# Performance work log

Hardware: AMD Instinct MI355X
Metric: run time of the kernel (lower is better)

Reference implementation:

```python
import jax, jax.numpy as jnp
import numpy as np

BRANCH = 8
DEPTH = 4
BATCH = 8192


def _build_tree(b=BRANCH, depth=DEPTH):
    level_sizes = [b ** l for l in range(depth + 1)]
    offsets = np.cumsum([0] + level_sizes)
    E = int(offsets[-1])  # 4681 total nodes (edges)
    parent = np.full(E, -1, dtype=np.int64)
    for l in range(1, depth + 1):
        idx = np.arange(level_sizes[l])
        parent[offsets[l] + idx] = offsets[l - 1] + idx // b
    # Each node's softmax group = its parent's children group; root -> group 0 ('ROOT').
    # Internal nodes occupy indices [0, offsets[depth]), so group id = parent+1.
    seg = np.where(parent < 0, 0, parent + 1).astype(np.int32)
    # path_onehot[i, j] = 1 iff j is an ancestor of i or i itself (path to root)
    P = np.zeros((E, E), dtype=np.float32)
    rows = np.arange(E)
    cur = rows.copy()
    for _ in range(depth + 1):
        P[rows, cur] = 1.0
        cur = np.where(parent[cur] < 0, cur, parent[cur])
    P[rows, cur] = 1.0  # root
    return seg, P


def setup_inputs() -> dict:
    key = jax.random.key(0)
    seg, P = _build_tree()
    E = seg.shape[0]
    inputs = jax.random.normal(key, (BATCH, E), dtype=jnp.float32)
    return {
        "inputs": inputs,
        "segment_ids": jnp.asarray(seg),
        "path_onehot": jnp.asarray(P),
    }


def _cascade_log_softmax(inputs, segment_ids, num_segments):
    # inputs: [B, E]; segmented (per-group) log_softmax along the edge axis.
    xT = inputs.T  # [E, B]
    mx = jax.ops.segment_max(xT, segment_ids, num_segments=num_segments)  # [S, B]
    shifted = xT - mx[segment_ids]
    lse = jnp.log(jax.ops.segment_sum(jnp.exp(shifted), segment_ids,
                                      num_segments=num_segments))  # [S, B]
    return (shifted - lse[segment_ids]).T  # [B, E]


def reference(inputs, segment_ids, path_onehot):
    # final_probabilities: product of conditionals along root-to-node paths
    num_segments = int(jnp.max(segment_ids)) + 1
    log_prob = _cascade_log_softmax(inputs, segment_ids, num_segments)  # [B, E]
    # log p(node) = sum of conditional log-probs over ancestors-or-self
    return jnp.exp(log_prob @ path_onehot.T)  # [B, E]
```

## Files before the change

kernel.cpp:

```cpp
#include <hip/hip_runtime.h>


constexpr int E     = 4681;
constexpr int NG    = 585;
constexpr int NSLOT = 5266;

__device__ __forceinline__ int xslot(int i) { return 9 * (i >> 3) + (i & 7); }

__device__ __forceinline__ void async_ld(const float* g, float* l) {
    __builtin_amdgcn_global_load_lds(
        (const __attribute__((address_space(1))) void*)g,
        (__attribute__((address_space(3))) void*)l, 4, 0, 0);
}

__device__ __forceinline__ float group_adj(const float w[8]) {
    float m = w[0];
    #pragma unroll
    for (int k = 1; k < 8; ++k) m = fmaxf(m, w[k]);
    float s = 0.0f;
    #pragma unroll
    for (int k = 0; k < 8; ++k) s += __expf(w[k] - m);
    return -m - __logf(s);
}

__device__ __forceinline__ void rdwin(const float* xs, int g, float w[8]) {
    const float* b = xs + 9 * g;
    #pragma unroll
    for (int k = 0; k < 7; ++k) w[k] = b[1 + k];
    w[7] = b[9];
}

__device__ __forceinline__ float walkD(const float* xs, int g, float adjv) {
    float D = adjv;
    if (g > 0) {
        const int p = (g - 1) >> 3;
        D += xs[xslot(g)] + xs[9 * p + 8];
        if (p > 0) {
            const int pp = (p - 1) >> 3;
            D += xs[xslot(p)] + xs[9 * pp + 8];
            if (pp > 0) D += xs[xslot(pp)] + xs[8];
        }
    }
    return D;
}

template<int S>
__device__ __forceinline__ void emit(float* __restrict__ rout, const float* xs,
                                     int g, float D) {
    float y[8];
    {
        const float* b = xs + 9 * g;
        #pragma unroll
        for (int k = 0; k < 7; ++k) y[k] = __expf(b[1 + k] + D);
        y[7] = __expf(b[9] + D);
    }
    float* q = rout + 8 * g + 1;
    if (S == 0) {
        *(float4*)(q)     = make_float4(y[0], y[1], y[2], y[3]);
        *(float4*)(q + 4) = make_float4(y[4], y[5], y[6], y[7]);
    } else if (S == 1) {
        q[0] = y[0];
        *(float2*)(q + 1) = make_float2(y[1], y[2]);
        *(float4*)(q + 3) = make_float4(y[3], y[4], y[5], y[6]);
        q[7] = y[7];
    } else if (S == 2) {
        *(float2*)(q)     = make_float2(y[0], y[1]);
        *(float4*)(q + 2) = make_float4(y[2], y[3], y[4], y[5]);
        *(float2*)(q + 6) = make_float2(y[6], y[7]);
    } else {
        q[0] = y[0];
        *(float4*)(q + 1) = make_float4(y[1], y[2], y[3], y[4]);
        *(float2*)(q + 5) = make_float2(y[5], y[6]);
        q[7] = y[7];
    }
}

template<int S>
__device__ __forceinline__ void row_body(const float* __restrict__ rin,
                                         float* __restrict__ rout,
                                         float* xs, int tid) {
    const int lbase = tid & ~63;
    #pragma unroll
    for (int j = 0; j < 21; ++j) {
        const int s = 256 * j + tid;
        if (s < NSLOT && (s % 9) != 8) {
            async_ld(rin + 8 * (s / 9) + (s % 9), xs + 256 * j + lbase);
        }
    }
    asm volatile("s_waitcnt vmcnt(0)" ::: "memory");
    __syncthreads();

    const int g0 = tid, g1 = tid + 256, g2 = tid + 512;
    const bool h2 = (g2 < NG);
    float w[8];
    rdwin(xs, g0, w);
    const float a0 = group_adj(w);
    rdwin(xs, g1, w);
    const float a1 = group_adj(w);
    float a2 = 0.f;
    if (h2) { rdwin(xs, g2, w); a2 = group_adj(w); }
    xs[9 * g0 + 8] = a0;
    xs[9 * g1 + 8] = a1;
    if (h2) xs[9 * g2 + 8] = a2;
    __syncthreads();

    emit<S>(rout, xs, g0, walkD(xs, g0, a0));
    emit<S>(rout, xs, g1, walkD(xs, g1, a1));
    if (h2) emit<S>(rout, xs, g2, walkD(xs, g2, a2));
    if (tid == 0) rout[0] = 1.0f;
}

__global__ __launch_bounds__(256, 7) void cascade_kernel(const float* __restrict__ in,
                                                         float* __restrict__ out) {
    __shared__ float xs[NSLOT];
    const int tid = threadIdx.x;
    const long long rowbase = (long long)blockIdx.x * (long long)E;
    const float* rin = in + rowbase;
    float* rout = out + rowbase;
    switch ((int)((rowbase + 1) & 3)) {
        case 0: row_body<0>(rin, rout, xs, tid); break;
        case 1: row_body<1>(rin, rout, xs, tid); break;
        case 2: row_body<2>(rin, rout, xs, tid); break;
        case 3: row_body<3>(rin, rout, xs, tid); break;
    }
}

extern "C" void kernel_launch(void* const* d_in, const int* in_sizes, int n_in,
                              void* d_out, int out_size, void* d_ws, size_t ws_size,
                              hipStream_t stream) {
    const float* in = (const float*)d_in[0];
    float* out = (float*)d_out;
    const int B = in_sizes[0] / E;
    cascade_kernel<<<B, 256, 0, stream>>>(in, out);
}
```

Baseline: 297.2 us.

## Use persistent blocks with double-buffered async LDS prefetch of next row

Switches from one block per row to a persistent grid of 768 blocks that loop over rows, staging the next row into a second LDS buffer while computing the current one. The goal is to hide global load latency and cut per-block launch overhead. The staging index arithmetic is now incremental and branch-free, using dummy loads for padding slots. It trades occupancy (launch bounds 7 to 3, double LDS) for overlap, and relies on vmcnt counting being correct. The store-alignment template is keyed on block id, which matches the row because GRID is a multiple of 4.

```diff
diff --git a/kernel.cpp b/kernel.cpp
--- a/kernel.cpp
+++ b/kernel.cpp
@@ -4,6 +4,8 @@
 constexpr int E     = 4681;
 constexpr int NG    = 585;
 constexpr int NSLOT = 5266;
+constexpr int BUF   = 5376;
+constexpr int GRID  = 768;
 
 __device__ __forceinline__ int xslot(int i) { return 9 * (i >> 3) + (i & 7); }
 
@@ -11,6 +13,22 @@
     __builtin_amdgcn_global_load_lds(
         (const __attribute__((address_space(1))) void*)g,
         (__attribute__((address_space(3))) void*)l, 4, 0, 0);
+}
+
+__device__ __forceinline__ void stage(const float* __restrict__ rin, float* xb,
+                                      int tid, int q0, int r0) {
+    const int lbase = tid & ~63;
+    int off = 8 * q0 + r0;
+    int r = r0;
+    #pragma unroll
+    for (int j = 0; j < 21; ++j) {
+        int a = (r == 8) ? (off - 1) : off;
+        if (j == 20) a = (tid < NSLOT - 5120) ? a : 0;
+        async_ld(rin + a, xb + 256 * j + lbase);
+        const bool wrap = (r >= 5);
+        off += wrap ? 227 : 228;
+        r   += wrap ? -5 : 4;
+    }
 }
 
 __device__ __forceinline__ float group_adj(const float w[8]) {
@@ -76,52 +94,61 @@
 }
 
 template<int S>
-__device__ __forceinline__ void row_body(const float* __restrict__ rin,
-                                         float* __restrict__ rout,
-                                         float* xs, int tid) {
-    const int lbase = tid & ~63;
-    #pragma unroll
-    for (int j = 0; j < 21; ++j) {
-        const int s = 256 * j + tid;
-        if (s < NSLOT && (s % 9) != 8) {
-            async_ld(rin + 8 * (s / 9) + (s % 9), xs + 256 * j + lbase);
-        }
-    }
-    asm volatile("s_waitcnt vmcnt(0)" ::: "memory");
-    __syncthreads();
-
+__device__ __forceinline__ void compute_row(float* xb, float* __restrict__ rout,
+                                            int tid) {
     const int g0 = tid, g1 = tid + 256, g2 = tid + 512;
     const bool h2 = (g2 < NG);
     float w[8];
-    rdwin(xs, g0, w);
-    const float a0 = group_adj(w);
-    rdwin(xs, g1, w);
-    const float a1 = group_adj(w);
+    rdwin(xb, g0, w); const float a0 = group_adj(w);
+    rdwin(xb, g1, w); const float a1 = group_adj(w);
     float a2 = 0.f;
-    if (h2) { rdwin(xs, g2, w); a2 = group_adj(w); }
-    xs[9 * g0 + 8] = a0;
-    xs[9 * g1 + 8] = a1;
-    if (h2) xs[9 * g2 + 8] = a2;
-    __syncthreads();
-
-    emit<S>(rout, xs, g0, walkD(xs, g0, a0));
-    emit<S>(rout, xs, g1, walkD(xs, g1, a1));
-    if (h2) emit<S>(rout, xs, g2, walkD(xs, g2, a2));
+    if (h2) { rdwin(xb, g2, w); a2 = group_adj(w); }
+    xb[9 * g0 + 8] = a0;
+    xb[9 * g1 + 8] = a1;
+    if (h2) xb[9 * g2 + 8] = a2;
+    asm volatile("s_waitcnt lgkmcnt(0)" ::: "memory");
+    __builtin_amdgcn_sched_barrier(0);
+    __builtin_amdgcn_s_barrier();
+    __builtin_amdgcn_sched_barrier(0);
+    emit<S>(rout, xb, g0, walkD(xb, g0, a0));
+    emit<S>(rout, xb, g1, walkD(xb, g1, a1));
+    if (h2) emit<S>(rout, xb, g2, walkD(xb, g2, a2));
     if (tid == 0) rout[0] = 1.0f;
 }
 
-__global__ __launch_bounds__(256, 7) void cascade_kernel(const float* __restrict__ in,
-                                                         float* __restrict__ out) {
-    __shared__ float xs[NSLOT];
+template<int S>
+__device__ __forceinline__ void run(const float* __restrict__ in,
+                                    float* __restrict__ out,
+                                    float* b0, float* b1, int tid, int bid, int B) {
+    const int q0 = tid / 9, r0 = tid % 9;
+    float* xb = b0;
+    float* xo = b1;
+    stage(in + (long long)bid * E, xb, tid, q0, r0);
+    for (int row = bid; row < B; row += GRID) {
+        if (row == bid) { asm volatile("s_waitcnt vmcnt(0)" ::: "memory"); }
+        else            { asm volatile("s_waitcnt vmcnt(4)" ::: "memory"); }
+        __builtin_amdgcn_sched_barrier(0);
+        __builtin_amdgcn_s_barrier();
+        __builtin_amdgcn_sched_barrier(0);
+        const int nxt = row + GRID;
+        if (nxt < B) stage(in + (long long)nxt * E, xo, tid, q0, r0);
+        __builtin_amdgcn_sched_barrier(0);
+        compute_row<S>(xb, out + (long long)row * E, tid);
+        float* t = xb; xb = xo; xo = t;
+    }
+}
+
+__global__ __launch_bounds__(256, 3) void cascade_kernel(const float* __restrict__ in,
+                                                         float* __restrict__ out,
+                                                         int B) {
+    __shared__ float b0[BUF], b1[BUF];
     const int tid = threadIdx.x;
-    const long long rowbase = (long long)blockIdx.x * (long long)E;
-    const float* rin = in + rowbase;
-    float* rout = out + rowbase;
-    switch ((int)((rowbase + 1) & 3)) {
-        case 0: row_body<0>(rin, rout, xs, tid); break;
-        case 1: row_body<1>(rin, rout, xs, tid); break;
-        case 2: row_body<2>(rin, rout, xs, tid); break;
-        case 3: row_body<3>(rin, rout, xs, tid); break;
+    const int bid = blockIdx.x;
+    switch ((bid + 1) & 3) {
+        case 0: run<0>(in, out, b0, b1, tid, bid, B); break;
+        case 1: run<1>(in, out, b0, b1, tid, bid, B); break;
+        case 2: run<2>(in, out, b0, b1, tid, bid, B); break;
+        case 3: run<3>(in, out, b0, b1, tid, bid, B); break;
     }
 }
 
@@ -131,5 +158,6 @@
     const float* in = (const float*)d_in[0];
     float* out = (float*)d_out;
     const int B = in_sizes[0] / E;
-    cascade_kernel<<<B, 256, 0, stream>>>(in, out);
+    const int grid = (B < GRID) ? B : GRID;
+    cascade_kernel<<<grid, 256, 0, stream>>>(in, out, B);
 }
```

Measured after the change: 297.9 us. No clear change (+0.2%).

## Process one row per wavefront with register windows instead of block-wide LDS staging

Applied to the files above, without the earlier changes.

Each 64-lane wavefront now handles a whole row. Child groups are read directly from global memory into registers using aligned float4 loads, and only the per-group log-sum-exp adjustments are kept in a small per-wave LDS array. The leaf groups are handled in a software-pipelined loop of eight steps, where the next group's window is prefetched while the current one is emitted. This drops the full-row LDS staging and the block-wide barriers, so LDS use falls sharply and memory traffic can overlap with compute. The cost is more register pressure and reliance on wave-synchronous LDS visibility, since there is only an lgkmcnt wait and no barrier.

```diff
diff --git a/kernel.cpp b/kernel.cpp
--- a/kernel.cpp
+++ b/kernel.cpp
@@ -1,16 +1,30 @@
 #include <hip/hip_runtime.h>
 
 
-constexpr int E     = 4681;
-constexpr int NG    = 585;
-constexpr int NSLOT = 5266;
+constexpr int E   = 4681;
+constexpr int ADP = 80;
 
-__device__ __forceinline__ int xslot(int i) { return 9 * (i >> 3) + (i & 7); }
-
-__device__ __forceinline__ void async_ld(const float* g, float* l) {
-    __builtin_amdgcn_global_load_lds(
-        (const __attribute__((address_space(1))) void*)g,
-        (__attribute__((address_space(3))) void*)l, 4, 0, 0);
+template<int S>
+__device__ __forceinline__ void loadwin(const float* __restrict__ rin, int g, float w[8]) {
+    if (g == 584) {
+        #pragma unroll
+        for (int k = 0; k < 8; ++k) w[k] = rin[4673 + k];
+        return;
+    }
+    const float* ap = rin + 8 * g + 1 - S;
+    float L[12];
+    const float4 A = *(const float4*)ap;
+    const float4 Bv = *(const float4*)(ap + 4);
+    L[0] = A.x;  L[1] = A.y;  L[2] = A.z;  L[3] = A.w;
+    L[4] = Bv.x; L[5] = Bv.y; L[6] = Bv.z; L[7] = Bv.w;
+    if (S != 0) {
+        const float4 Cv = *(const float4*)(ap + 8);
+        L[8] = Cv.x; L[9] = Cv.y; L[10] = Cv.z; L[11] = Cv.w;
+    } else {
+        L[8] = L[9] = L[10] = L[11] = 0.0f;
+    }
+    #pragma unroll
+    for (int k = 0; k < 8; ++k) w[k] = L[S + k];
 }
 
 __device__ __forceinline__ float group_adj(const float w[8]) {
@@ -23,37 +37,12 @@
     return -m - __logf(s);
 }
 
-__device__ __forceinline__ void rdwin(const float* xs, int g, float w[8]) {
-    const float* b = xs + 9 * g;
+template<int S>
+__device__ __forceinline__ void emit(float* __restrict__ rout, int g,
+                                     const float w[8], float D) {
+    float y[8];
     #pragma unroll
-    for (int k = 0; k < 7; ++k) w[k] = b[1 + k];
-    w[7] = b[9];
-}
-
-__device__ __forceinline__ float walkD(const float* xs, int g, float adjv) {
-    float D = adjv;
-    if (g > 0) {
-        const int p = (g - 1) >> 3;
-        D += xs[xslot(g)] + xs[9 * p + 8];
-        if (p > 0) {
-            const int pp = (p - 1) >> 3;
-            D += xs[xslot(p)] + xs[9 * pp + 8];
-            if (pp > 0) D += xs[xslot(pp)] + xs[8];
-        }
-    }
-    return D;
-}
-
-template<int S>
-__device__ __forceinline__ void emit(float* __restrict__ rout, const float* xs,
-                                     int g, float D) {
-    float y[8];
-    {
-        const float* b = xs + 9 * g;
-        #pragma unroll
-        for (int k = 0; k < 7; ++k) y[k] = __expf(b[1 + k] + D);
-        y[7] = __expf(b[9] + D);
-    }
+    for (int k = 0; k < 8; ++k) y[k] = __expf(w[k] + D);
     float* q = rout + 8 * g + 1;
     if (S == 0) {
         *(float4*)(q)     = make_float4(y[0], y[1], y[2], y[3]);
@@ -75,53 +64,91 @@
     }
 }
 
-template<int S>
-__device__ __forceinline__ void row_body(const float* __restrict__ rin,
-                                         float* __restrict__ rout,
-                                         float* xs, int tid) {
-    const int lbase = tid & ~63;
-    #pragma unroll
-    for (int j = 0; j < 21; ++j) {
-        const int s = 256 * j + tid;
-        if (s < NSLOT && (s % 9) != 8) {
-            async_ld(rin + 8 * (s / 9) + (s % 9), xs + 256 * j + lbase);
-        }
+template<int S, int C>
+__device__ __forceinline__ void step3(const float* __restrict__ rin,
+                                      float* __restrict__ rout,
+                                      const float* __restrict__ AD, float AD0,
+                                      int l, const float w[8], float xg,
+                                      float wn[8], float& xn) {
+    if (C < 7) {
+        const int gn = 73 + 64 * (C + 1) + l;
+        loadwin<S>(rin, gn, wn);
+        xn = rin[gn];
     }
-    asm volatile("s_waitcnt vmcnt(0)" ::: "memory");
-    __syncthreads();
-
-    const int g0 = tid, g1 = tid + 256, g2 = tid + 512;
-    const bool h2 = (g2 < NG);
-    float w[8];
-    rdwin(xs, g0, w);
-    const float a0 = group_adj(w);
-    rdwin(xs, g1, w);
-    const float a1 = group_adj(w);
-    float a2 = 0.f;
-    if (h2) { rdwin(xs, g2, w); a2 = group_adj(w); }
-    xs[9 * g0 + 8] = a0;
-    xs[9 * g1 + 8] = a1;
-    if (h2) xs[9 * g2 + 8] = a2;
-    __syncthreads();
-
-    emit<S>(rout, xs, g0, walkD(xs, g0, a0));
-    emit<S>(rout, xs, g1, walkD(xs, g1, a1));
-    if (h2) emit<S>(rout, xs, g2, walkD(xs, g2, a2));
-    if (tid == 0) rout[0] = 1.0f;
+    const int g = 73 + 64 * C + l;
+    const float adj = group_adj(w);
+    const float D = xg + adj + AD[9 + 8 * C + (l >> 3)] + AD[C + 1] + AD0;
+    emit<S>(rout, g, w, D);
 }
 
-__global__ __launch_bounds__(256, 7) void cascade_kernel(const float* __restrict__ in,
-                                                         float* __restrict__ out) {
-    __shared__ float xs[NSLOT];
+template<int S>
+__device__ __forceinline__ void wave_row(const float* __restrict__ rin,
+                                         float* __restrict__ rout,
+                                         float* __restrict__ AD, int l) {
+    float wA[8], wB[8];
+    float xB = 0.0f;
+    loadwin<S>(rin, l, wA);
+    const float xA = rin[l];
+    const bool hB = (l < 9);
+    if (hB) { loadwin<S>(rin, 64 + l, wB); xB = rin[64 + l]; }
+
+    const float adjA = group_adj(wA);
+    const float ADa = (l == 0) ? adjA : (xA + adjA);
+    AD[l] = ADa;
+    float ADb = 0.0f;
+    if (hB) { ADb = xB + group_adj(wB); AD[64 + l] = ADb; }
+    #pragma unroll
+    for (int k = 0; k < 8; ++k) {
+        asm volatile("" : "+v"(wA[k]));
+        asm volatile("" : "+v"(wB[k]));
+    }
+    asm volatile("s_waitcnt lgkmcnt(0)" ::: "memory");
+
+    const float AD0 = AD[0];
+    {
+        float D;
+        if (l == 0) D = ADa;
+        else {
+            const int p = (l - 1) >> 3;
+            D = ADa + AD[p] + ((p > 0) ? AD0 : 0.0f);
+        }
+        emit<S>(rout, l, wA, D);
+    }
+    if (l == 0) rout[0] = 1.0f;
+    if (hB) {
+        const int p = (63 + l) >> 3;
+        emit<S>(rout, 64 + l, wB, ADb + AD[p] + AD0);
+    }
+
+    float w0[8], w1[8], x0, x1 = 0.0f;
+    loadwin<S>(rin, 73 + l, w0);
+    x0 = rin[73 + l];
+    step3<S, 0>(rin, rout, AD, AD0, l, w0, x0, w1, x1);
+    step3<S, 1>(rin, rout, AD, AD0, l, w1, x1, w0, x0);
+    step3<S, 2>(rin, rout, AD, AD0, l, w0, x0, w1, x1);
+    step3<S, 3>(rin, rout, AD, AD0, l, w1, x1, w0, x0);
+    step3<S, 4>(rin, rout, AD, AD0, l, w0, x0, w1, x1);
+    step3<S, 5>(rin, rout, AD, AD0, l, w1, x1, w0, x0);
+    step3<S, 6>(rin, rout, AD, AD0, l, w0, x0, w1, x1);
+    step3<S, 7>(rin, rout, AD, AD0, l, w1, x1, w0, x0);
+}
+
+__global__ __launch_bounds__(256, 6) void cascade_kernel(const float* __restrict__ in,
+                                                         float* __restrict__ out,
+                                                         int B) {
+    __shared__ float ADs[4 * ADP];
     const int tid = threadIdx.x;
-    const long long rowbase = (long long)blockIdx.x * (long long)E;
-    const float* rin = in + rowbase;
-    float* rout = out + rowbase;
-    switch ((int)((rowbase + 1) & 3)) {
-        case 0: row_body<0>(rin, rout, xs, tid); break;
-        case 1: row_body<1>(rin, rout, xs, tid); break;
-        case 2: row_body<2>(rin, rout, xs, tid); break;
-        case 3: row_body<3>(rin, rout, xs, tid); break;
+    const int wv = tid >> 6, l = tid & 63;
+    const int row = blockIdx.x * 4 + wv;
+    if (row >= B) return;
+    const float* rin = in + (long long)row * E;
+    float* rout = out + (long long)row * E;
+    float* AD = ADs + wv * ADP;
+    switch ((row + 1) & 3) {
+        case 0: wave_row<0>(rin, rout, AD, l); break;
+        case 1: wave_row<1>(rin, rout, AD, l); break;
+        case 2: wave_row<2>(rin, rout, AD, l); break;
+        case 3: wave_row<3>(rin, rout, AD, l); break;
     }
 }
 
@@ -131,5 +158,6 @@
     const float* in = (const float*)d_in[0];
     float* out = (float*)d_out;
     const int B = in_sizes[0] / E;
-    cascade_kernel<<<B, 256, 0, stream>>>(in, out);
+    const int grid = (B + 3) / 4;
+    cascade_kernel<<<grid, 256, 0, stream>>>(in, out, B);
 }
```

Measured after the change: 307.7 us. +3.5%, slower.
